# Kernel optimization log

Measured on AMD Instinct MI355X. Metric: run time of the kernel, lower is better.

## Reference

```python
import jax, jax.numpy as jnp
import numpy as np
from jax import lax

ALPHA = 0.99  # get_norm_alpha(8000, 80, 1.0): exp(-0.01)=0.99005 -> rounds to 0.99 (<1)
B, C, T, F = 64, 2, 4000, 96


def setup_inputs() -> dict:
    key = jax.random.key(0)
    k1, = jax.random.split(key, 1)
    feat_spec = jax.random.normal(k1, (B, C, T, F), dtype=jnp.float32)
    # make_spec_norm_state(): linspace(unit_norm_init_start, unit_norm_init_end, df_bins)
    state = jnp.linspace(0.001, 0.0001, F, dtype=jnp.float32)[None, None, :]  # [1,1,F]
    return {"feat_spec": feat_spec, "state": state}


def reference(feat_spec, state):
    b, c, t, f = feat_spec.shape
    state0 = jnp.broadcast_to(state, (b, 1, f)).astype(feat_spec.dtype)

    def step(s, x):  # x: [b, c, f], s: [b, 1, f]
        abs2 = jnp.sum(x * x, axis=1, keepdims=True)          # [b, 1, f]
        new_s = abs2 * (1.0 - ALPHA) + s * ALPHA              # EMA of |X|^2
        y = x / jnp.sqrt(new_s)                               # RMS-style norm
        return new_s, y

    xs = jnp.moveaxis(feat_spec, 2, 0)                        # [t, b, c, f]
    final_state, ys = lax.scan(step, state0, xs)
    out = jnp.moveaxis(ys, 0, 2)                              # [b, c, t, f]
    return out, final_state
```

## Files before the change

### kernel.cpp

```cpp
#include <hip/hip_runtime.h>


namespace {
constexpr int Bdim = 64, Cdim = 2, Tdim = 4000, Fdim = 96;
constexpr int K = 50, L = 80;
constexpr int FG = Fdim / 4;
constexpr int CHAINS = Bdim * FG;
constexpr float kAlpha = 0.99f;
constexpr float kOneMinusAlpha = 0.01f;
constexpr float kAlphaL = 0.447523215f;

typedef float v4f __attribute__((ext_vector_type(4)));

__device__ __forceinline__ v4f ld4(const float* p) {
  return *reinterpret_cast<const v4f*>(p);
}
}

__global__ __launch_bounds__(256) void spec_ema_phase1(
    const float* __restrict__ x, float* __restrict__ bws) {
  const int g = blockIdx.x * 256 + threadIdx.x;
  const int chain = g % CHAINS;
  const int k = g / CHAINS;
  const int b = chain / FG, fg = chain % FG;

  const size_t base =
      ((size_t)b * Cdim * Tdim + (size_t)k * L) * Fdim + (size_t)fg * 4;
  const float* p0 = x + base;
  const float* p1 = p0 + (size_t)Tdim * Fdim;

  v4f s = 0.0f;
#pragma unroll 4
  for (int j = 0; j < L; ++j) {
    v4f x0 = ld4(p0 + (size_t)j * Fdim);
    v4f x1 = ld4(p1 + (size_t)j * Fdim);
    v4f abs2 = x0 * x0 + x1 * x1;
    s = s * kAlpha + abs2 * kOneMinusAlpha;
  }
  *reinterpret_cast<v4f*>(bws + (size_t)g * 4) = s;
}

__global__ __launch_bounds__(256) void spec_ema_phase3(
    const float* __restrict__ x, const float* __restrict__ state,
    const float* __restrict__ bws, float* __restrict__ out) {
  const int g = blockIdx.x * 256 + threadIdx.x;
  const int chain = g % CHAINS;
  const int k = g / CHAINS;
  const int b = chain / FG, fg = chain % FG;

  v4f s = ld4(state + (size_t)fg * 4);
  for (int m = 0; m < k; ++m) {
    v4f bm = ld4(bws + ((size_t)m * CHAINS + chain) * 4);
    s = s * kAlphaL + bm;
  }

  const size_t base =
      ((size_t)b * Cdim * Tdim + (size_t)k * L) * Fdim + (size_t)fg * 4;
  const float* p0 = x + base;
  const float* p1 = p0 + (size_t)Tdim * Fdim;
  float* q0 = out + base;
  float* q1 = q0 + (size_t)Tdim * Fdim;

#pragma unroll 4
  for (int j = 0; j < L; ++j) {
    v4f x0 = ld4(p0 + (size_t)j * Fdim);
    v4f x1 = ld4(p1 + (size_t)j * Fdim);
    v4f abs2 = x0 * x0 + x1 * x1;
    s = s * kAlpha + abs2 * kOneMinusAlpha;
    v4f r;
    r.x = rsqrtf(s.x);
    r.y = rsqrtf(s.y);
    r.z = rsqrtf(s.z);
    r.w = rsqrtf(s.w);
    v4f y0 = x0 * r;
    v4f y1 = x1 * r;
    __builtin_nontemporal_store(y0, reinterpret_cast<v4f*>(q0 + (size_t)j * Fdim));
    __builtin_nontemporal_store(y1, reinterpret_cast<v4f*>(q1 + (size_t)j * Fdim));
  }

  if (k == K - 1) {
    *reinterpret_cast<v4f*>(out + (size_t)Bdim * Cdim * Tdim * Fdim +
                            (size_t)b * Fdim + (size_t)fg * 4) = s;
  }
}

extern "C" void kernel_launch(void* const* d_in, const int* in_sizes, int n_in,
                              void* d_out, int out_size, void* d_ws, size_t ws_size,
                              hipStream_t stream) {
  const float* x = (const float*)d_in[0];
  const float* state = (const float*)d_in[1];
  float* out = (float*)d_out;
  float* bws = (float*)d_ws;

  spec_ema_phase1<<<CHAINS * (K - 1) / 256, 256, 0, stream>>>(x, bws);
  spec_ema_phase3<<<CHAINS * K / 256, 256, 0, stream>>>(x, state, bws, out);
}
```

Baseline: 384.9 us.

## Add separate carry-scan kernel and split time into more, shorter chunks

Adds a middle kernel that turns each chain's per-chunk partial EMA sums into chunk-start states through one sequential prefix pass, written back in place. Phase 3 no longer replays all earlier chunks per thread. The chunk count goes from 50 to 200 and chunk length from 80 to 20, so there are more parallel threads and a shorter serial recurrence per thread. The cost is a third launch and a sequential 199-step loop in phase 2 that runs on only 1536 threads.

New measurement: 397.6 us. +3.3%, slower.

```diff
diff --git a/kernel.cpp b/kernel.cpp
--- a/kernel.cpp
+++ b/kernel.cpp
@@ -3,17 +3,20 @@
 
 namespace {
 constexpr int Bdim = 64, Cdim = 2, Tdim = 4000, Fdim = 96;
-constexpr int K = 50, L = 80;
+constexpr int K = 200, L = 20;
 constexpr int FG = Fdim / 4;
 constexpr int CHAINS = Bdim * FG;
 constexpr float kAlpha = 0.99f;
 constexpr float kOneMinusAlpha = 0.01f;
-constexpr float kAlphaL = 0.447523215f;
+constexpr float kAlphaL = 0.8179069376f;
 
 typedef float v4f __attribute__((ext_vector_type(4)));
 
 __device__ __forceinline__ v4f ld4(const float* p) {
   return *reinterpret_cast<const v4f*>(p);
+}
+__device__ __forceinline__ void st4(float* p, v4f v) {
+  *reinterpret_cast<v4f*>(p) = v;
 }
 }
 
@@ -30,29 +33,41 @@
   const float* p1 = p0 + (size_t)Tdim * Fdim;
 
   v4f s = 0.0f;
-#pragma unroll 4
+#pragma unroll 5
   for (int j = 0; j < L; ++j) {
     v4f x0 = ld4(p0 + (size_t)j * Fdim);
     v4f x1 = ld4(p1 + (size_t)j * Fdim);
     v4f abs2 = x0 * x0 + x1 * x1;
     s = s * kAlpha + abs2 * kOneMinusAlpha;
   }
-  *reinterpret_cast<v4f*>(bws + (size_t)g * 4) = s;
+  st4(bws + (size_t)g * 4, s);
+}
+
+__global__ __launch_bounds__(256) void spec_ema_phase2(
+    const float* __restrict__ state, float* __restrict__ bws) {
+  const int chain = blockIdx.x * 256 + threadIdx.x;
+  const int fg = chain % FG;
+
+  v4f p = ld4(state + (size_t)fg * 4);
+#pragma unroll 4
+  for (int m = 0; m < K - 1; ++m) {
+    float* slot = bws + ((size_t)m * CHAINS + chain) * 4;
+    v4f bm = ld4(slot);
+    st4(slot, p);
+    p = p * kAlphaL + bm;
+  }
+  st4(bws + ((size_t)(K - 1) * CHAINS + chain) * 4, p);
 }
 
 __global__ __launch_bounds__(256) void spec_ema_phase3(
-    const float* __restrict__ x, const float* __restrict__ state,
-    const float* __restrict__ bws, float* __restrict__ out) {
+    const float* __restrict__ x, const float* __restrict__ bws,
+    float* __restrict__ out) {
   const int g = blockIdx.x * 256 + threadIdx.x;
   const int chain = g % CHAINS;
   const int k = g / CHAINS;
   const int b = chain / FG, fg = chain % FG;
 
-  v4f s = ld4(state + (size_t)fg * 4);
-  for (int m = 0; m < k; ++m) {
-    v4f bm = ld4(bws + ((size_t)m * CHAINS + chain) * 4);
-    s = s * kAlphaL + bm;
-  }
+  v4f s = ld4(bws + (size_t)g * 4);
 
   const size_t base =
       ((size_t)b * Cdim * Tdim + (size_t)k * L) * Fdim + (size_t)fg * 4;
@@ -61,7 +76,7 @@
   float* q0 = out + base;
   float* q1 = q0 + (size_t)Tdim * Fdim;
 
-#pragma unroll 4
+#pragma unroll 5
   for (int j = 0; j < L; ++j) {
     v4f x0 = ld4(p0 + (size_t)j * Fdim);
     v4f x1 = ld4(p1 + (size_t)j * Fdim);
@@ -72,15 +87,14 @@
     r.y = rsqrtf(s.y);
     r.z = rsqrtf(s.z);
     r.w = rsqrtf(s.w);
-    v4f y0 = x0 * r;
-    v4f y1 = x1 * r;
-    __builtin_nontemporal_store(y0, reinterpret_cast<v4f*>(q0 + (size_t)j * Fdim));
-    __builtin_nontemporal_store(y1, reinterpret_cast<v4f*>(q1 + (size_t)j * Fdim));
+    __builtin_nontemporal_store(x0 * r, reinterpret_cast<v4f*>(q0 + (size_t)j * Fdim));
+    __builtin_nontemporal_store(x1 * r, reinterpret_cast<v4f*>(q1 + (size_t)j * Fdim));
   }
 
   if (k == K - 1) {
-    *reinterpret_cast<v4f*>(out + (size_t)Bdim * Cdim * Tdim * Fdim +
-                            (size_t)b * Fdim + (size_t)fg * 4) = s;
+    st4(out + (size_t)Bdim * Cdim * Tdim * Fdim + (size_t)b * Fdim +
+            (size_t)fg * 4,
+        s);
   }
 }
 
@@ -93,5 +107,6 @@
   float* bws = (float*)d_ws;
 
   spec_ema_phase1<<<CHAINS * (K - 1) / 256, 256, 0, stream>>>(x, bws);
-  spec_ema_phase3<<<CHAINS * K / 256, 256, 0, stream>>>(x, state, bws, out);
+  spec_ema_phase2<<<CHAINS / 256, 256, 0, stream>>>(state, bws);
+  spec_ema_phase3<<<CHAINS * K / 256, 256, 0, stream>>>(x, bws, out);
 }
```
